# Kernel tuning notes

Measured on AMD Instinct MI355X. Metric: run time of the kernel, lower is better.

Reference implementation:

```python
import jax, jax.numpy as jnp
import numpy as np

CHUNK = 128  # single steady-state chunk tier (T divisible by 128)
DECAY_MIN = 0.005


def setup_inputs() -> dict:
    key = jax.random.key(0)
    k0, k1, k2, k3, k4 = jax.random.split(key, 5)
    B, H, T, K = 4, 16, 2048, 64
    r = jax.random.normal(k0, (B, H, T, K), jnp.float32) * 0.5
    k = jax.random.normal(k1, (B, H, T, K), jnp.float32) * 0.5
    v = jax.random.normal(k2, (B, H, T, K), jnp.float32)
    # log-space decay (negative); mild magnitude keeps exp() of cumulative
    # in-chunk decays within fp32 range (torch original upcasts to fp64)
    w = -(jax.random.uniform(k3, (B, H, T, K), jnp.float32) * 0.2 + 0.01)
    u = jax.random.normal(k4, (1, H, 1, K), jnp.float32) * 0.5
    wkv_state = jnp.zeros((B, H, K, K), jnp.float32)
    return {"r": r, "k": k, "v": v, "w": w, "u": u, "wkv_state": wkv_state}


def _chunked_wkv(r, k, v, w, u, wkv_state):
    B, H, T, K = r.shape
    Tc = CHUNK
    N = T // Tc
    # decay preprocessing (log space)
    w_decay = jnp.clip(jnp.exp(w), DECAY_MIN, None)
    w_log = jnp.log(w_decay)
    wc = w_log.reshape(B, H, N, Tc, K)
    wc_cum = jnp.cumsum(wc, axis=-2)                       # inclusive cumsum
    shifted = jnp.pad(wc_cum[..., :-1, :], ((0, 0), (0, 0), (0, 0), (1, 0), (0, 0)))
    ws = wc.sum(axis=-2, keepdims=True)                    # (B,H,N,1,K)
    w_inter = jnp.exp(ws - wc_cum)                          # (B,H,N,Tc,K)
    w_intra = jnp.exp(wc_cum - wc)
    ws_e = jnp.exp(jnp.swapaxes(ws, -1, -2))               # (B,H,N,K,1)

    rc = r.reshape(B, H, N, Tc, K)
    kc = k.reshape(B, H, N, Tc, K)
    vc = v.reshape(B, H, N, Tc, K)

    # numerically-centered intra-chunk decays (offset at chunk midpoint)
    off = shifted[..., Tc // 2:Tc // 2 + 1, :]
    r_dec = jnp.exp(shifted - off)
    k_inv = jnp.exp(off - wc_cum)

    # intra-chunk attention: strictly-lower-triangular + u-bonus diagonal
    a = jnp.einsum('bhnik,bhnjk->bhnij', rc * r_dec, kc * k_inv)
    a = jnp.tril(a, -1)
    diag = jnp.einsum('bhntk,bhntk->bhnt', rc, u[:, :, None] * kc)
    a = a + diag[..., :, None] * jnp.eye(Tc, dtype=a.dtype)
    out = jnp.einsum('bhnij,bhnjv->bhniv', a, vc)

    # inter-chunk: sequential state carry via scan
    wkv = jnp.einsum('bhntk,bhntv->bhnkv', kc * w_inter, vc)   # (B,H,N,K,K)

    def step(state, inp):
        ws_i, wkv_i = inp
        return state * ws_i + wkv_i, state

    ws_s = jnp.moveaxis(ws_e, 2, 0)    # (N,B,H,K,1)
    wkv_s = jnp.moveaxis(wkv, 2, 0)    # (N,B,H,K,K)
    final_state, states = jax.lax.scan(step, wkv_state, (ws_s, wkv_s))
    states = jnp.moveaxis(states, 0, 2)  # (B,H,N,K,K) — state entering chunk n

    out = out + jnp.einsum('bhntk,bhnkv->bhntv', rc * w_intra, states)
    return out.reshape(B, H, T, K), final_state


def reference(r, k, v, w, u, wkv_state):
    return _chunked_wkv(r, k, v, w, u, wkv_state)
```

## Files before the change

### kernel.cpp

```cpp
#include <hip/hip_runtime.h>

#define TC 128
#define KD 64
#define WLOG_MIN (-5.2983174f)

typedef __attribute__((ext_vector_type(8))) short short8;
typedef __attribute__((ext_vector_type(4))) short short4_t;
typedef __attribute__((ext_vector_type(4))) float f32x4;

__device__ __forceinline__ unsigned short f2bf(float x) {
  union { float f; unsigned int u; } c; c.f = x;
  unsigned int u = c.u + 0x7fffu + ((c.u >> 16) & 1u);
  return (unsigned short)(u >> 16);
}
__device__ __forceinline__ float bf2f(unsigned short x) {
  union { unsigned int u; float f; } c; c.u = ((unsigned int)x) << 16; return c.f;
}


__global__ __launch_bounds__(256, 3)
void rwkv_intra_mfma(const float* __restrict__ rr, const float* __restrict__ kk_,
                     const float* __restrict__ vv, const float* __restrict__ ww,
                     const float* __restrict__ uu, float* __restrict__ out,
                     unsigned short* __restrict__ wkv_u16, float* __restrict__ wse_ws,
                     unsigned short* __restrict__ rw_u16, unsigned short* __restrict__ diag_u16,
                     int H, int N) {
  __shared__ alignas(16) unsigned short rd_s[TC * KD];
  __shared__ alignas(16) unsigned short ki_s[TC * KD];
  __shared__ alignas(16) unsigned short vT_s[KD * TC];
  __shared__ alignas(16) unsigned char su_raw[5120];
  float* segtot = (float*)su_raw;
  unsigned short* Ast = (unsigned short*)su_raw;

  const int bid = blockIdx.x;
  const int n = bid % N, bh = bid / N, h = bh % H;
  const size_t base = ((size_t)bh * N + n) * (TC * KD);
  const float *rg = rr + base, *kg = kk_ + base, *vg = vv + base, *wg = ww + base;
  unsigned short* diagg = diag_u16 + (size_t)bid * TC;

  const int tid = threadIdx.x;
  const int lk = tid & 63;
  const int wv = tid >> 6;

  float wl[32];
  {
    float c = 0.f;
    #pragma unroll
    for (int tt = 0; tt < 32; ++tt) {
      wl[tt] = fmaxf(wg[(wv * 32 + tt) * KD + lk], WLOG_MIN);
      c += wl[tt];
    }
    segtot[wv * 64 + lk] = c;
  }
  __syncthreads();
  const float s0 = segtot[0 * 64 + lk], s1 = segtot[1 * 64 + lk];
  const float s2 = segtot[2 * 64 + lk], s3 = segtot[3 * 64 + lk];
  const float myoff = s0 + s1;
  const float segofs = (wv == 0) ? 0.f : (wv == 1) ? s0 : (wv == 2) ? (s0 + s1) : (s0 + s1 + s2);
  const float wsum = s0 + s1 + s2 + s3;
  const float wsoff_own = __expf(wsum - myoff);
  if (wv == 0) wse_ws[((size_t)bh * N + n) * KD + lk] = __expf(wsum);
  const float eoff = __expf(myoff);

  {
    float c = segofs;
    const float uk = uu[h * KD + lk];
    unsigned short* rwg = rw_u16 + base;
    short8 vb8;
    float darr[8];
    #pragma unroll
    for (int tt = 0; tt < 32; ++tt) {
      const int t = wv * 32 + tt;
      float rv = rg[t * KD + lk], kv = kg[t * KD + lk], vvv = vg[t * KD + lk];
      const int slot = (lk >> 3) ^ (t & 7) ^ ((t >> 3) & 7);
      const int nat = t * KD + (slot << 3) + (lk & 7);
      float e1 = __expf(c - myoff);
      rd_s[nat] = f2bf(rv * e1);
      rwg[t * KD + lk] = f2bf(rv * e1 * eoff);
      ki_s[nat] = f2bf(kv * __expf(myoff - c - wl[tt]));
      vb8[tt & 7] = (short)f2bf(vvv);
      darr[tt & 7] = rv * uk * kv;
      c += wl[tt];
      if ((tt & 7) == 7) {
        const int g = t >> 3;
        *(short8*)&vT_s[lk * TC + ((g ^ (lk & 7)) << 3)] = vb8;
        #pragma unroll
        for (int o = 32; o > 0; o >>= 1)
          #pragma unroll
          for (int q = 0; q < 8; ++q) darr[q] += __shfl_xor(darr[q], o, 64);
        if (lk == 0) {
          short8 dpk;
          #pragma unroll
          for (int q = 0; q < 8; ++q) dpk[q] = (short)f2bf(darr[q]);
          *(short8*)&diagg[g * 8] = dpk;
        }
      }
    }
  }
  __syncthreads();

  const int lane = tid & 63, quad = lane >> 4, l16 = lane & 15;

  {
    f32x4 acc[4] = {{0,0,0,0},{0,0,0,0},{0,0,0,0},{0,0,0,0}};
    const int kdg = wv * 2 + (l16 >> 3), kd7 = l16 & 7;
    #pragma unroll
    for (int ks = 0; ks < 4; ++ks) {
      short8 a;
      #pragma unroll
      for (int j = 0; j < 8; ++j) {
        const int t = ks * 32 + quad * 8 + j;
        a[j] = (short)ki_s[t * KD + (((kdg ^ (t & 7) ^ ((t >> 3) & 7)) << 3) + kd7)];
      }
      #pragma unroll
      for (int nn = 0; nn < 4; ++nn) {
        const int vd = nn * 16 + l16;
        short8 b = *(const short8*)&vT_s[vd * TC + (((ks * 4 + quad) ^ (vd & 7)) << 3)];
        acc[nn] = __builtin_amdgcn_mfma_f32_16x16x32_bf16(a, b, acc[nn], 0, 0, 0);
      }
    }
    float wso[4];
    #pragma unroll
    for (int reg = 0; reg < 4; ++reg) wso[reg] = __shfl(wsoff_own, wv * 16 + quad * 4 + reg, 64);
    unsigned short* wkvg = wkv_u16 + ((size_t)bh * N + n) * (KD * KD);
    #pragma unroll
    for (int nn = 0; nn < 4; ++nn)
      #pragma unroll
      for (int reg = 0; reg < 4; ++reg)
        wkvg[(wv * 16 + quad * 4 + reg) * KD + nn * 16 + l16] = f2bf(acc[nn][reg] * wso[reg]);
  }

  #pragma unroll
  for (int half = 0; half < 2; ++half) {
    const int ib = half ? (7 - wv) : wv;
    const int i0 = ib * 16;
    const int irow = i0 + l16;
    const int rsw = (irow & 7) ^ ((irow >> 3) & 7);
    short8 b0 = *(const short8*)&rd_s[irow * KD + ((quad ^ rsw) << 3)];
    short8 b1 = *(const short8*)&rd_s[irow * KD + (((4 + quad) ^ rsw) << 3)];
    const float diag_i = bf2f(diagg[irow]);
    f32x4 oacc[4] = {{0,0,0,0},{0,0,0,0},{0,0,0,0},{0,0,0,0}};
    const int npairs = (ib + 2) >> 1;
    unsigned short* astw = Ast + wv * 640;
    for (int jp = 0; jp < npairs; ++jp) {
      #pragma unroll
      for (int jj = 0; jj < 2; ++jj) {
        const int j = jp * 2 + jj;
        short4_t pk;
        if (j <= ib) {
          const int jrow = j * 16 + l16;
          const int jsw = (jrow & 7) ^ ((jrow >> 3) & 7);
          short8 a0 = *(const short8*)&ki_s[jrow * KD + ((quad ^ jsw) << 3)];
          short8 a1 = *(const short8*)&ki_s[jrow * KD + (((4 + quad) ^ jsw) << 3)];
          f32x4 at = {0, 0, 0, 0};
          at = __builtin_amdgcn_mfma_f32_16x16x32_bf16(a0, b0, at, 0, 0, 0);
          at = __builtin_amdgcn_mfma_f32_16x16x32_bf16(a1, b1, at, 0, 0, 0);
          #pragma unroll
          for (int reg = 0; reg < 4; ++reg) {
            const int je = j * 16 + quad * 4 + reg;
            float val = at[reg];
            if (j == ib) val = (je < irow) ? val : ((je == irow) ? diag_i : 0.f);
            pk[reg] = (short)f2bf(val);
          }
        } else {
          pk = (short4_t)0;
        }
        *(short4_t*)&astw[l16 * 40 + jj * 16 + quad * 4] = pk;
      }
      short8 af = *(const short8*)&astw[l16 * 40 + quad * 8];
      #pragma unroll
      for (int nn = 0; nn < 4; ++nn) {
        const int vd = nn * 16 + l16;
        short8 bv = *(const short8*)&vT_s[vd * TC + (((jp * 4 + quad) ^ (vd & 7)) << 3)];
        oacc[nn] = __builtin_amdgcn_mfma_f32_16x16x32_bf16(af, bv, oacc[nn], 0, 0, 0);
      }
    }
    float* og = out + base;
    #pragma unroll
    for (int nn = 0; nn < 4; ++nn)
      #pragma unroll
      for (int reg = 0; reg < 4; ++reg)
        og[(i0 + quad * 4 + reg) * KD + nn * 16 + l16] = oacc[nn][reg];
  }
}

__global__ __launch_bounds__(256)
void rwkv_scan_inter(const unsigned short* __restrict__ wkv_u16,
                     const float* __restrict__ wse_ws,
                     const float* __restrict__ st_in,
                     const unsigned short* __restrict__ rw_u16,
                     float* __restrict__ out, float* __restrict__ final_out, int N) {
  __shared__ alignas(16) unsigned short sT[16 * KD];
  const int bh = blockIdx.x >> 2, vq = blockIdx.x & 3;
  const int tid = threadIdx.x;
  const int vd_l = tid & 15;
  const int kd0 = (tid >> 4) * 4;
  const size_t sbase = (size_t)bh * (KD * KD);

  float stt[4];
  #pragma unroll
  for (int j = 0; j < 4; ++j) stt[j] = st_in[sbase + (kd0 + j) * KD + vq * 16 + vd_l];

  float nwk[4], nwe[4];
  #pragma unroll
  for (int j = 0; j < 4; ++j) {
    nwk[j] = bf2f(wkv_u16[(size_t)bh * N * (KD * KD) + (kd0 + j) * KD + vq * 16 + vd_l]);
    nwe[j] = wse_ws[(size_t)bh * N * KD + kd0 + j];
  }

  const int lane = tid & 63, wv = tid >> 6, quad = lane >> 4, l16 = lane & 15;
  for (int n = 0; n < N; ++n) {
    #pragma unroll
    for (int j = 0; j < 4; ++j) {
      const int kd = kd0 + j;
      sT[vd_l * KD + ((((kd >> 3) ^ (vd_l & 7)) << 3) | (kd & 7))] = f2bf(stt[j]);
    }
    __syncthreads();

    float cwk[4], cwe[4];
    #pragma unroll
    for (int j = 0; j < 4; ++j) { cwk[j] = nwk[j]; cwe[j] = nwe[j]; }
    if (n + 1 < N) {
      const size_t b2 = (size_t)bh * N + n + 1;
      #pragma unroll
      for (int j = 0; j < 4; ++j) {
        nwk[j] = bf2f(wkv_u16[b2 * (KD * KD) + (kd0 + j) * KD + vq * 16 + vd_l]);
        nwe[j] = wse_ws[b2 * KD + kd0 + j];
      }
    }

    const unsigned short* rwg = rw_u16 + ((size_t)bh * N + n) * (TC * KD);
    float* og = out + ((size_t)bh * N + n) * (TC * KD);
    #pragma unroll
    for (int half = 0; half < 2; ++half) {
      const int mt = wv + half * 4;
      const int trow = mt * 16 + l16;
      short8 a0 = *(const short8*)&rwg[trow * KD + quad * 8];
      short8 a1 = *(const short8*)&rwg[trow * KD + 32 + quad * 8];
      short8 b0 = *(const short8*)&sT[l16 * KD + ((quad ^ (l16 & 7)) << 3)];
      short8 b1 = *(const short8*)&sT[l16 * KD + (((4 + quad) ^ (l16 & 7)) << 3)];
      f32x4 acc = {0, 0, 0, 0};
      acc = __builtin_amdgcn_mfma_f32_16x16x32_bf16(a0, b0, acc, 0, 0, 0);
      acc = __builtin_amdgcn_mfma_f32_16x16x32_bf16(a1, b1, acc, 0, 0, 0);
      #pragma unroll
      for (int reg = 0; reg < 4; ++reg) {
        const size_t oi = (size_t)(mt * 16 + quad * 4 + reg) * KD + vq * 16 + l16;
        og[oi] += acc[reg];
      }
    }

    #pragma unroll
    for (int j = 0; j < 4; ++j) stt[j] = stt[j] * cwe[j] + cwk[j];
    __syncthreads();
  }
  #pragma unroll
  for (int j = 0; j < 4; ++j)
    final_out[sbase + (kd0 + j) * KD + vq * 16 + vd_l] = stt[j];
}

extern "C" void kernel_launch(void* const* d_in, const int* in_sizes, int n_in,
                              void* d_out, int out_size, void* d_ws, size_t ws_size,
                              hipStream_t stream) {
  const float* r = (const float*)d_in[0];
  const float* k = (const float*)d_in[1];
  const float* v = (const float*)d_in[2];
  const float* w = (const float*)d_in[3];
  const float* u = (const float*)d_in[4];
  const float* st0 = (const float*)d_in[5];
  float* out = (float*)d_out;

  const int BH = in_sizes[5] / (KD * KD);
  const int H = in_sizes[4] / KD;
  const int T = in_sizes[0] / (BH * KD);
  const int N = T / TC;

  unsigned short* wkv_u16 = (unsigned short*)d_ws;
  float* wse_ws = (float*)(wkv_u16 + (size_t)BH * N * KD * KD);
  unsigned short* rw_u16 = (unsigned short*)(wse_ws + (size_t)BH * N * KD);
  unsigned short* diag_u16 = rw_u16 + (size_t)BH * T * KD;
  float* final_out = out + (size_t)in_sizes[0];

  rwkv_intra_mfma<<<BH * N, 256, 0, stream>>>(r, k, v, w, u, out, wkv_u16, wse_ws,
                                              rw_u16, diag_u16, H, N);
  rwkv_scan_inter<<<BH * 4, 256, 0, stream>>>(wkv_u16, wse_ws, st0, rw_u16,
                                              out, final_out, N);
}
```

Baseline: 205.3 us.

## Split inter-chunk scan into state-only scan and parallel apply kernel

The sequential scan kernel now only propagates the chunk states. It writes each chunk's incoming state as bf16 into the wkv workspace, reusing slots that have already been read. A new kernel, launched over all (batch·head, chunk) pairs, applies r·w_intra times the state with MFMA and accumulates into the output. This moves the matmul and output read-modify-write off the serial chain so they run with full grid parallelism. The cost is an extra launch and a global round trip for the states.

```diff
diff --git a/kernel.cpp b/kernel.cpp
--- a/kernel.cpp
+++ b/kernel.cpp
@@ -185,21 +185,19 @@
 }
 
 __global__ __launch_bounds__(256)
-void rwkv_scan_inter(const unsigned short* __restrict__ wkv_u16,
-                     const float* __restrict__ wse_ws,
-                     const float* __restrict__ st_in,
-                     const unsigned short* __restrict__ rw_u16,
-                     float* __restrict__ out, float* __restrict__ final_out, int N) {
-  __shared__ alignas(16) unsigned short sT[16 * KD];
+void rwkv_scan_states(const float* __restrict__ wse_ws,
+                      const float* __restrict__ st_in,
+                      unsigned short* __restrict__ wkv_u16,
+                      float* __restrict__ final_out, int N) {
   const int bh = blockIdx.x >> 2, vq = blockIdx.x & 3;
   const int tid = threadIdx.x;
-  const int vd_l = tid & 15;
-  const int kd0 = (tid >> 4) * 4;
+  const int vd_l = tid & 15, kd0 = (tid >> 4) * 4;
   const size_t sbase = (size_t)bh * (KD * KD);
 
   float stt[4];
   #pragma unroll
-  for (int j = 0; j < 4; ++j) stt[j] = st_in[sbase + (kd0 + j) * KD + vq * 16 + vd_l];
+  for (int j = 0; j < 4; ++j)
+    stt[j] = st_in[sbase + (kd0 + j) * KD + vq * 16 + vd_l];
 
   float nwk[4], nwe[4];
   #pragma unroll
@@ -208,15 +206,7 @@
     nwe[j] = wse_ws[(size_t)bh * N * KD + kd0 + j];
   }
 
-  const int lane = tid & 63, wv = tid >> 6, quad = lane >> 4, l16 = lane & 15;
   for (int n = 0; n < N; ++n) {
-    #pragma unroll
-    for (int j = 0; j < 4; ++j) {
-      const int kd = kd0 + j;
-      sT[vd_l * KD + ((((kd >> 3) ^ (vd_l & 7)) << 3) | (kd & 7))] = f2bf(stt[j]);
-    }
-    __syncthreads();
-
     float cwk[4], cwe[4];
     #pragma unroll
     for (int j = 0; j < 4; ++j) { cwk[j] = nwk[j]; cwe[j] = nwe[j]; }
@@ -228,34 +218,68 @@
         nwe[j] = wse_ws[b2 * KD + kd0 + j];
       }
     }
-
-    const unsigned short* rwg = rw_u16 + ((size_t)bh * N + n) * (TC * KD);
-    float* og = out + ((size_t)bh * N + n) * (TC * KD);
-    #pragma unroll
-    for (int half = 0; half < 2; ++half) {
-      const int mt = wv + half * 4;
-      const int trow = mt * 16 + l16;
-      short8 a0 = *(const short8*)&rwg[trow * KD + quad * 8];
-      short8 a1 = *(const short8*)&rwg[trow * KD + 32 + quad * 8];
-      short8 b0 = *(const short8*)&sT[l16 * KD + ((quad ^ (l16 & 7)) << 3)];
-      short8 b1 = *(const short8*)&sT[l16 * KD + (((4 + quad) ^ (l16 & 7)) << 3)];
+    __syncthreads();
+    unsigned short* sg = wkv_u16 + ((size_t)bh * N + n) * (KD * KD);
+    #pragma unroll
+    for (int j = 0; j < 4; ++j)
+      sg[(kd0 + j) * KD + vq * 16 + vd_l] = f2bf(stt[j]);
+    #pragma unroll
+    for (int j = 0; j < 4; ++j) stt[j] = stt[j] * cwe[j] + cwk[j];
+  }
+  #pragma unroll
+  for (int j = 0; j < 4; ++j)
+    final_out[sbase + (kd0 + j) * KD + vq * 16 + vd_l] = stt[j];
+}
+
+__global__ __launch_bounds__(256)
+void rwkv_apply_inter(const unsigned short* __restrict__ st_u16,
+                      const unsigned short* __restrict__ rw_u16,
+                      float* __restrict__ out, int N) {
+  __shared__ alignas(16) unsigned short sT[KD * KD];
+  const int bid = blockIdx.x;
+  const int n = bid % N, bh = bid / N;
+  const int tid = threadIdx.x;
+
+  {
+    const unsigned short* sg = st_u16 + ((size_t)bh * N + n) * (KD * KD);
+    const int kd = tid >> 2, v0 = (tid & 3) * 16;
+    short8 x0 = *(const short8*)&sg[kd * KD + v0];
+    short8 x1 = *(const short8*)&sg[kd * KD + v0 + 8];
+    const int g = kd >> 3, k7 = kd & 7;
+    #pragma unroll
+    for (int i = 0; i < 8; ++i) {
+      int vd = v0 + i;
+      sT[vd * KD + (((g ^ (vd & 7)) << 3) | k7)] = (unsigned short)x0[i];
+      vd = v0 + 8 + i;
+      sT[vd * KD + (((g ^ (vd & 7)) << 3) | k7)] = (unsigned short)x1[i];
+    }
+  }
+  __syncthreads();
+
+  const int lane = tid & 63, wv = tid >> 6, quad = lane >> 4, l16 = lane & 15;
+  const unsigned short* rwg = rw_u16 + ((size_t)bh * N + n) * (TC * KD);
+  float* og = out + ((size_t)bh * N + n) * (TC * KD);
+  #pragma unroll
+  for (int half = 0; half < 2; ++half) {
+    const int mt = wv + half * 4;
+    const int trow = mt * 16 + l16;
+    short8 a0 = *(const short8*)&rwg[trow * KD + quad * 8];
+    short8 a1 = *(const short8*)&rwg[trow * KD + 32 + quad * 8];
+    #pragma unroll
+    for (int nn = 0; nn < 4; ++nn) {
+      const int vd = nn * 16 + l16;
+      short8 b0 = *(const short8*)&sT[vd * KD + ((quad ^ (vd & 7)) << 3)];
+      short8 b1 = *(const short8*)&sT[vd * KD + (((4 + quad) ^ (vd & 7)) << 3)];
       f32x4 acc = {0, 0, 0, 0};
       acc = __builtin_amdgcn_mfma_f32_16x16x32_bf16(a0, b0, acc, 0, 0, 0);
       acc = __builtin_amdgcn_mfma_f32_16x16x32_bf16(a1, b1, acc, 0, 0, 0);
       #pragma unroll
       for (int reg = 0; reg < 4; ++reg) {
-        const size_t oi = (size_t)(mt * 16 + quad * 4 + reg) * KD + vq * 16 + l16;
+        const size_t oi = (size_t)(mt * 16 + quad * 4 + reg) * KD + nn * 16 + l16;
         og[oi] += acc[reg];
       }
     }
-
-    #pragma unroll
-    for (int j = 0; j < 4; ++j) stt[j] = stt[j] * cwe[j] + cwk[j];
-    __syncthreads();
-  }
-  #pragma unroll
-  for (int j = 0; j < 4; ++j)
-    final_out[sbase + (kd0 + j) * KD + vq * 16 + vd_l] = stt[j];
+  }
 }
 
 extern "C" void kernel_launch(void* const* d_in, const int* in_sizes, int n_in,
@@ -282,6 +306,6 @@
 
   rwkv_intra_mfma<<<BH * N, 256, 0, stream>>>(r, k, v, w, u, out, wkv_u16, wse_ws,
                                               rw_u16, diag_u16, H, N);
-  rwkv_scan_inter<<<BH * 4, 256, 0, stream>>>(wkv_u16, wse_ws, st0, rw_u16,
-                                              out, final_out, N);
-}
+  rwkv_scan_states<<<BH * 4, 256, 0, stream>>>(wse_ws, st0, wkv_u16, final_out, N);
+  rwkv_apply_inter<<<BH * N, 256, 0, stream>>>(wkv_u16, rw_u16, out, N);
+}
```

After: 203.4 us. No clear change (-0.9%).

## Parallelize inter-chunk scan across chunks by recomputing prefix state per block

Applied to the files above, without the earlier changes.

Replaces the sequential per-(b,h) scan kernel, which launched only BH*4 blocks and looped over all N chunks, with one block per (bh, chunk). Each block recomputes its incoming state by replaying the recurrence over the earlier chunks, then applies it with MFMA. The output update is staged in shared memory so the global read-modify-write of out uses coalesced vector loads. The cost is redundant O(N^2) state recurrence work and more reads of the wkv buffers, in exchange for many more blocks in flight.

```diff
diff --git a/kernel.cpp b/kernel.cpp
--- a/kernel.cpp
+++ b/kernel.cpp
@@ -184,78 +184,112 @@
   }
 }
 
-__global__ __launch_bounds__(256)
-void rwkv_scan_inter(const unsigned short* __restrict__ wkv_u16,
+__global__ __launch_bounds__(256, 6)
+void rwkv_scan_apply(const unsigned short* __restrict__ wkv_u16,
                      const float* __restrict__ wse_ws,
                      const float* __restrict__ st_in,
                      const unsigned short* __restrict__ rw_u16,
                      float* __restrict__ out, float* __restrict__ final_out, int N) {
-  __shared__ alignas(16) unsigned short sT[16 * KD];
-  const int bh = blockIdx.x >> 2, vq = blockIdx.x & 3;
+  __shared__ alignas(16) unsigned short sT[KD * KD];
+  __shared__ alignas(16) float obuf[64 * 68];
+
+  const int bid = blockIdx.x;
+  const int n = bid % N, bh = bid / N;
   const int tid = threadIdx.x;
-  const int vd_l = tid & 15;
-  const int kd0 = (tid >> 4) * 4;
+
+  const int kd = tid >> 2, v0 = (tid & 3) * 16;
   const size_t sbase = (size_t)bh * (KD * KD);
-
-  float stt[4];
+  float s[16];
   #pragma unroll
-  for (int j = 0; j < 4; ++j) stt[j] = st_in[sbase + (kd0 + j) * KD + vq * 16 + vd_l];
-
-  float nwk[4], nwe[4];
+  for (int i = 0; i < 16; i += 4)
+    *(f32x4*)&s[i] = *(const f32x4*)&st_in[sbase + kd * KD + v0 + i];
+
+  const float* wseb = wse_ws + (size_t)bh * N * KD + kd;
+  const unsigned short* wkvb = wkv_u16 + (size_t)bh * N * (KD * KD) + kd * KD + v0;
+
+  {
+    float e_c = 0.f; short8 x0_c = {0}, x1_c = {0};
+    if (n > 0) {
+      e_c = wseb[0];
+      x0_c = *(const short8*)&wkvb[0];
+      x1_c = *(const short8*)&wkvb[8];
+    }
+    for (int j = 0; j < n; ++j) {
+      const float e = e_c; const short8 x0 = x0_c, x1 = x1_c;
+      if (j + 1 < n) {
+        e_c = wseb[(size_t)(j + 1) * KD];
+        x0_c = *(const short8*)&wkvb[(size_t)(j + 1) * (KD * KD)];
+        x1_c = *(const short8*)&wkvb[(size_t)(j + 1) * (KD * KD) + 8];
+      }
+      #pragma unroll
+      for (int i = 0; i < 8; ++i) {
+        s[i]     = s[i]     * e + bf2f((unsigned short)x0[i]);
+        s[i + 8] = s[i + 8] * e + bf2f((unsigned short)x1[i]);
+      }
+    }
+  }
+
+  {
+    const int g = kd >> 3, k7 = kd & 7;
+    #pragma unroll
+    for (int i = 0; i < 16; ++i) {
+      const int vd = v0 + i;
+      sT[vd * KD + (((g ^ (vd & 7)) << 3) | k7)] = f2bf(s[i]);
+    }
+  }
+
+  if (n == N - 1) {
+    const float e = wseb[(size_t)(N - 1) * KD];
+    const short8 x0 = *(const short8*)&wkvb[(size_t)(N - 1) * (KD * KD)];
+    const short8 x1 = *(const short8*)&wkvb[(size_t)(N - 1) * (KD * KD) + 8];
+    #pragma unroll
+    for (int i = 0; i < 8; ++i) {
+      s[i]     = s[i]     * e + bf2f((unsigned short)x0[i]);
+      s[i + 8] = s[i + 8] * e + bf2f((unsigned short)x1[i]);
+    }
+    #pragma unroll
+    for (int i = 0; i < 16; i += 4)
+      *(f32x4*)&final_out[sbase + kd * KD + v0 + i] = *(const f32x4*)&s[i];
+  }
+  __syncthreads();
+
+  const int lane = tid & 63, wv = tid >> 6, quad = lane >> 4, l16 = lane & 15;
+  const unsigned short* rwg = rw_u16 + ((size_t)bh * N + n) * (TC * KD);
+  float* og = out + ((size_t)bh * N + n) * (TC * KD);
   #pragma unroll
-  for (int j = 0; j < 4; ++j) {
-    nwk[j] = bf2f(wkv_u16[(size_t)bh * N * (KD * KD) + (kd0 + j) * KD + vq * 16 + vd_l]);
-    nwe[j] = wse_ws[(size_t)bh * N * KD + kd0 + j];
-  }
-
-  const int lane = tid & 63, wv = tid >> 6, quad = lane >> 4, l16 = lane & 15;
-  for (int n = 0; n < N; ++n) {
-    #pragma unroll
-    for (int j = 0; j < 4; ++j) {
-      const int kd = kd0 + j;
-      sT[vd_l * KD + ((((kd >> 3) ^ (vd_l & 7)) << 3) | (kd & 7))] = f2bf(stt[j]);
-    }
-    __syncthreads();
-
-    float cwk[4], cwe[4];
-    #pragma unroll
-    for (int j = 0; j < 4; ++j) { cwk[j] = nwk[j]; cwe[j] = nwe[j]; }
-    if (n + 1 < N) {
-      const size_t b2 = (size_t)bh * N + n + 1;
-      #pragma unroll
-      for (int j = 0; j < 4; ++j) {
-        nwk[j] = bf2f(wkv_u16[b2 * (KD * KD) + (kd0 + j) * KD + vq * 16 + vd_l]);
-        nwe[j] = wse_ws[b2 * KD + kd0 + j];
-      }
-    }
-
-    const unsigned short* rwg = rw_u16 + ((size_t)bh * N + n) * (TC * KD);
-    float* og = out + ((size_t)bh * N + n) * (TC * KD);
-    #pragma unroll
-    for (int half = 0; half < 2; ++half) {
-      const int mt = wv + half * 4;
-      const int trow = mt * 16 + l16;
-      short8 a0 = *(const short8*)&rwg[trow * KD + quad * 8];
-      short8 a1 = *(const short8*)&rwg[trow * KD + 32 + quad * 8];
-      short8 b0 = *(const short8*)&sT[l16 * KD + ((quad ^ (l16 & 7)) << 3)];
-      short8 b1 = *(const short8*)&sT[l16 * KD + (((4 + quad) ^ (l16 & 7)) << 3)];
+  for (int half = 0; half < 2; ++half) {
+    const int mt = wv + half * 4;
+    const int trow = mt * 16 + l16;
+    short8 a0 = *(const short8*)&rwg[trow * KD + quad * 8];
+    short8 a1 = *(const short8*)&rwg[trow * KD + 32 + quad * 8];
+    const int lr0 = (mt - half * 4) * 16 + quad * 4;
+    #pragma unroll
+    for (int nn = 0; nn < 4; ++nn) {
+      const int vd = nn * 16 + l16;
+      short8 b0 = *(const short8*)&sT[vd * KD + ((quad ^ (vd & 7)) << 3)];
+      short8 b1 = *(const short8*)&sT[vd * KD + (((4 + quad) ^ (vd & 7)) << 3)];
       f32x4 acc = {0, 0, 0, 0};
       acc = __builtin_amdgcn_mfma_f32_16x16x32_bf16(a0, b0, acc, 0, 0, 0);
       acc = __builtin_amdgcn_mfma_f32_16x16x32_bf16(a1, b1, acc, 0, 0, 0);
       #pragma unroll
-      for (int reg = 0; reg < 4; ++reg) {
-        const size_t oi = (size_t)(mt * 16 + quad * 4 + reg) * KD + vq * 16 + l16;
-        og[oi] += acc[reg];
-      }
-    }
-
-    #pragma unroll
-    for (int j = 0; j < 4; ++j) stt[j] = stt[j] * cwe[j] + cwk[j];
+      for (int reg = 0; reg < 4; ++reg)
+        obuf[(lr0 + reg) * 68 + nn * 16 + l16] = acc[reg];
+    }
     __syncthreads();
-  }
-  #pragma unroll
-  for (int j = 0; j < 4; ++j)
-    final_out[sbase + (kd0 + j) * KD + vq * 16 + vd_l] = stt[j];
+    {
+      float* ogh = og + half * 64 * KD;
+      #pragma unroll
+      for (int i = 0; i < 4; ++i) {
+        const int f = tid + i * 256;
+        const int row = f >> 4, c4 = (f & 15) * 4;
+        f32x4 l = *(const f32x4*)&obuf[row * 68 + c4];
+        f32x4 gv = *(const f32x4*)&ogh[row * KD + c4];
+        gv += l;
+        *(f32x4*)&ogh[row * KD + c4] = gv;
+      }
+    }
+    __syncthreads();
+  }
 }
 
 extern "C" void kernel_launch(void* const* d_in, const int* in_sizes, int n_in,
@@ -282,6 +316,6 @@
 
   rwkv_intra_mfma<<<BH * N, 256, 0, stream>>>(r, k, v, w, u, out, wkv_u16, wse_ws,
                                               rw_u16, diag_u16, H, N);
-  rwkv_scan_inter<<<BH * 4, 256, 0, stream>>>(wkv_u16, wse_ws, st0, rw_u16,
+  rwkv_scan_apply<<<BH * N, 256, 0, stream>>>(wkv_u16, wse_ws, st0, rw_u16,
                                               out, final_out, N);
 }
```

New measurement: 198.5 us. -3.3%, faster.
